# Kernel tuning notes

Hardware: AMD Instinct MI355X
Metric: run time of the kernel (lower is better)

Reference implementation:

```python
import jax, jax.numpy as jnp
import numpy as np

D_MODEL = 1024
N_HEADS = 16
HEAD_DIM = D_MODEL // N_HEADS
D_FF = 4 * D_MODEL


def _layernorm(x, g, b, eps=1e-5):
    mu = jnp.mean(x, axis=-1, keepdims=True)
    var = jnp.var(x, axis=-1, keepdims=True)
    return (x - mu) * jax.lax.rsqrt(var + eps) * g + b


def setup_inputs() -> dict:
    key = jax.random.key(0)
    ks = jax.random.split(key, 12)
    s = lambda fan_in: 1.0 / np.sqrt(fan_in)
    x = jax.random.normal(ks[0], (2, 2048, D_MODEL), dtype=jnp.float32)
    return {
        "x": x,
        "ln1_g": jnp.ones((D_MODEL,), jnp.float32),
        "ln1_b": jnp.zeros((D_MODEL,), jnp.float32),
        "w_qkv": jax.random.uniform(ks[1], (D_MODEL, 3 * D_MODEL), jnp.float32, -s(D_MODEL), s(D_MODEL)),
        "b_qkv": jax.random.uniform(ks[2], (3 * D_MODEL,), jnp.float32, -s(D_MODEL), s(D_MODEL)),
        "w_out": jax.random.uniform(ks[3], (D_MODEL, D_MODEL), jnp.float32, -s(D_MODEL), s(D_MODEL)),
        "b_out": jax.random.uniform(ks[4], (D_MODEL,), jnp.float32, -s(D_MODEL), s(D_MODEL)),
        "ln2_g": jnp.ones((D_MODEL,), jnp.float32),
        "ln2_b": jnp.zeros((D_MODEL,), jnp.float32),
        "w_ff1": jax.random.uniform(ks[5], (D_MODEL, D_FF), jnp.float32, -s(D_MODEL), s(D_MODEL)),
        "b_ff1": jax.random.uniform(ks[6], (D_FF,), jnp.float32, -s(D_MODEL), s(D_MODEL)),
        "w_ff2": jax.random.uniform(ks[7], (D_FF, D_MODEL), jnp.float32, -s(D_FF), s(D_FF)),
        "b_ff2": jax.random.uniform(ks[8], (D_MODEL,), jnp.float32, -s(D_FF), s(D_FF)),
    }


def reference(x, ln1_g, ln1_b, w_qkv, b_qkv, w_out, b_out,
              ln2_g, ln2_b, w_ff1, b_ff1, w_ff2, b_ff2):
    B, T, C = x.shape
    # --- pre-LN causal self-attention + residual ---
    h = _layernorm(x, ln1_g, ln1_b)
    qkv = h @ w_qkv + b_qkv                                  # [B,T,3C]
    qkv = qkv.reshape(B, T, 3, N_HEADS, HEAD_DIM)
    q, k, v = qkv[:, :, 0], qkv[:, :, 1], qkv[:, :, 2]       # [B,T,H,Dh]
    scores = jnp.einsum("bthd,bshd->bhts", q, k) / np.sqrt(HEAD_DIM).astype(np.float32)
    causal = jnp.tril(jnp.ones((T, T), dtype=bool))
    scores = jnp.where(causal, scores, -jnp.inf)
    weights = jax.nn.softmax(scores, axis=-1)                # [B,H,T,T]
    attn = jnp.einsum("bhts,bshd->bthd", weights, v).reshape(B, T, C)
    x = x + attn @ w_out + b_out
    # --- pre-LN GELU FFN + residual ---
    h = _layernorm(x, ln2_g, ln2_b)
    h = jax.nn.gelu(h @ w_ff1 + b_ff1, approximate=False)    # torch GELU = erf
    x = x + h @ w_ff2 + b_ff2
    return x
```

## Files before the change

### kernel.cpp

```cpp
#include <hip/hip_runtime.h>
#include <hip/hip_bf16.h>
#include <math.h>

#define TSEQ 2048
#define BATCH 2
#define CDIM 1024
#define NH 16
#define HD 64
#define DFF 4096
#define ROWS (BATCH*TSEQ)

typedef __attribute__((ext_vector_type(4))) float f32x4;
typedef __attribute__((ext_vector_type(8))) short bf16x8;
typedef __attribute__((ext_vector_type(4))) unsigned short u16x4;

__device__ __forceinline__ void gload_lds16(const void* g, void* l) {
    void* gv = const_cast<void*>(g);
    __builtin_amdgcn_global_load_lds((__attribute__((address_space(1))) void*)gv,
                                     (__attribute__((address_space(3))) void*)l, 16, 0, 0);
}

__device__ __forceinline__ unsigned short f2bf(float f) {
    unsigned int u = __float_as_uint(f);
    return (unsigned short)((u + 0x7FFFu + ((u >> 16) & 1u)) >> 16);
}
__device__ __forceinline__ float bf2f(unsigned short u) {
    return __uint_as_float((unsigned int)u << 16);
}
__device__ __forceinline__ unsigned int cvt_pk_bf16(float lo, float hi) {
    unsigned int r;
    asm("v_cvt_pk_bf16_f32 %0, %1, %2" : "=v"(r) : "v"(lo), "v"(hi));
    return r;
}
__device__ __forceinline__ float fast_gelu(float v) {
    float u = fmaf(0.044715f * v * v, v, v);
    float e = __expf(-1.5957691216057308f * u);
    return v * __builtin_amdgcn_rcpf(1.0f + e);
}

__global__ __launch_bounds__(256) void ln_kernel(const float* __restrict__ x,
                                                 const float* __restrict__ g,
                                                 const float* __restrict__ b,
                                                 unsigned short* __restrict__ out) {
    int row = blockIdx.x;
    int tid = threadIdx.x;
    const float* xr = x + (size_t)row * CDIM;
    float4 v = *(const float4*)(xr + tid * 4);
    float s  = v.x + v.y + v.z + v.w;
    float s2 = v.x*v.x + v.y*v.y + v.z*v.z + v.w*v.w;
    #pragma unroll
    for (int off = 32; off >= 1; off >>= 1) {
        s  += __shfl_down(s, off);
        s2 += __shfl_down(s2, off);
    }
    __shared__ float red[8];
    int wid = tid >> 6, lane = tid & 63;
    if (lane == 0) { red[wid] = s; red[wid + 4] = s2; }
    __syncthreads();
    float ts  = red[0] + red[1] + red[2] + red[3];
    float ts2 = red[4] + red[5] + red[6] + red[7];
    float mu  = ts * (1.0f / CDIM);
    float var = ts2 * (1.0f / CDIM) - mu * mu;
    float rstd = rsqrtf(var + 1e-5f);
    float4 gv = *(const float4*)(g + tid * 4);
    float4 bv = *(const float4*)(b + tid * 4);
    unsigned short o4[4];
    o4[0] = f2bf((v.x - mu) * rstd * gv.x + bv.x);
    o4[1] = f2bf((v.y - mu) * rstd * gv.y + bv.y);
    o4[2] = f2bf((v.z - mu) * rstd * gv.z + bv.z);
    o4[3] = f2bf((v.w - mu) * rstd * gv.w + bv.w);
    *(u16x4*)(out + (size_t)row * CDIM + tid * 4) = *(u16x4*)o4;
}

__global__ __launch_bounds__(256) void prep_kernel(
        const float* __restrict__ w_qkv, const float* __restrict__ w_out,
        const float* __restrict__ w_ff1, const float* __restrict__ w_ff2,
        const float* __restrict__ x, const float* __restrict__ ln1_g,
        const float* __restrict__ ln1_b,
        unsigned short* __restrict__ wqkvT, unsigned short* __restrict__ woutT,
        unsigned short* __restrict__ wff1T, unsigned short* __restrict__ wff2T,
        unsigned short* __restrict__ h_bf) {
    __shared__ float T[64][65];
    __shared__ float red[8];
    int bid = blockIdx.x;
    int tid = threadIdx.x;

    if (bid >= 3072) {
        const int row = bid - 3072;
        const float* xr = x + (size_t)row * CDIM;
        float4 v = *(const float4*)(xr + tid * 4);
        float s  = v.x + v.y + v.z + v.w;
        float s2 = v.x*v.x + v.y*v.y + v.z*v.z + v.w*v.w;
        #pragma unroll
        for (int off = 32; off >= 1; off >>= 1) {
            s  += __shfl_down(s, off);
            s2 += __shfl_down(s2, off);
        }
        int wid = tid >> 6, lane = tid & 63;
        if (lane == 0) { red[wid] = s; red[wid + 4] = s2; }
        __syncthreads();
        float ts  = red[0] + red[1] + red[2] + red[3];
        float ts2 = red[4] + red[5] + red[6] + red[7];
        float mu  = ts * (1.0f / CDIM);
        float var = ts2 * (1.0f / CDIM) - mu * mu;
        float rstd = rsqrtf(var + 1e-5f);
        float4 gv = *(const float4*)(ln1_g + tid * 4);
        float4 bv = *(const float4*)(ln1_b + tid * 4);
        unsigned short o4[4];
        o4[0] = f2bf((v.x - mu) * rstd * gv.x + bv.x);
        o4[1] = f2bf((v.y - mu) * rstd * gv.y + bv.y);
        o4[2] = f2bf((v.z - mu) * rstd * gv.z + bv.z);
        o4[3] = f2bf((v.w - mu) * rstd * gv.w + bv.w);
        *(u16x4*)(h_bf + (size_t)row * CDIM + tid * 4) = *(u16x4*)o4;
        return;
    }

    const float* W; unsigned short* Wt; int K, N, nbx;
    if (bid < 768)       {             W = w_qkv; Wt = wqkvT; K = 1024; N = 3072; nbx = 48; }
    else if (bid < 1024) { bid -= 768;  W = w_out; Wt = woutT; K = 1024; N = 1024; nbx = 16; }
    else if (bid < 2048) { bid -= 1024; W = w_ff1; Wt = wff1T; K = 1024; N = 4096; nbx = 64; }
    else                 { bid -= 2048; W = w_ff2; Wt = wff2T; K = 4096; N = 1024; nbx = 16; }
    const int n0 = (bid % nbx) * 64, k0 = (bid / nbx) * 64;

    int kr = tid >> 4;
    int nc = (tid & 15) * 4;
    #pragma unroll
    for (int i = 0; i < 4; ++i) {
        float4 v = *(const float4*)&W[(size_t)(k0 + kr + i*16) * N + (n0 + nc)];
        T[kr + i*16][nc + 0] = v.x;
        T[kr + i*16][nc + 1] = v.y;
        T[kr + i*16][nc + 2] = v.z;
        T[kr + i*16][nc + 3] = v.w;
    }
    __syncthreads();
    int n  = tid >> 2;
    int kb = (tid & 3) * 16;
    unsigned short tmp[16];
    #pragma unroll
    for (int i = 0; i < 16; ++i) tmp[i] = f2bf(T[kb + i][n]);
    unsigned short* dst = Wt + (size_t)(n0 + n) * K + (k0 + kb);
    *(int4*)dst       = *(int4*)&tmp[0];
    *(int4*)(dst + 8) = *(int4*)&tmp[8];
}

template<int EPI>
__global__ __launch_bounds__(512) void gemm_kernel(const unsigned short* __restrict__ A,
                                                   const unsigned short* __restrict__ Bt,
                                                   const float* __restrict__ bias,
                                                   const float* __restrict__ res,
                                                   void* __restrict__ Cout,
                                                   unsigned short* __restrict__ kfrag_,
                                                   unsigned short* __restrict__ vfrag_,
                                                   int M, int N, int K,
                                                   int nxc, int xcw, int xrw) {
    __shared__ __align__(16) unsigned short As[3 * 8192];
    __shared__ __align__(16) unsigned short Bs[3 * 8192];
    const int tid = threadIdx.x;
    const int l   = tid & 63;
    const int w   = tid >> 6;
    const int wr  = (w >> 2) * 128;
    const int wcl = (w & 3) * 64;
    const int lin = blockIdx.x;
    const int xcd = lin & 7;
    const int idx = lin >> 3;
    const int xc  = xcd % nxc, xr = xcd / nxc;
    const long brow = (long)(xr * xrw + idx / xcw) * 256;
    const long bcol = (long)(xc * xcw + idx % xcw) * 256;

    const int srow = tid >> 2;
    const int schk = ((tid & 3) ^ ((srow >> 1) & 3)) * 8;
    const unsigned short* gA = A  + (size_t)(brow + srow) * K + schk;
    const unsigned short* gB = Bt + (size_t)(bcol + srow) * K + schk;

    f32x4 acc[8][4];
    #pragma unroll
    for (int m = 0; m < 8; ++m)
        #pragma unroll
        for (int n = 0; n < 4; ++n) acc[m][n] = (f32x4){0.f, 0.f, 0.f, 0.f};

    #define STAGE256(buf, koff_)                                                       \
        do {                                                                           \
            unsigned short* lA_ = As + (buf) * 8192 + tid * 8;                         \
            unsigned short* lB_ = Bs + (buf) * 8192 + tid * 8;                         \
            gload_lds16(gA + (koff_), lA_);                                            \
            gload_lds16(gA + (size_t)128 * K + (koff_), lA_ + 4096);                   \
            gload_lds16(gB + (koff_), lB_);                                            \
            gload_lds16(gB + (size_t)128 * K + (koff_), lB_ + 4096);                   \
        } while (0)

    STAGE256(0, 0);
    STAGE256(1, 32);

    int cur = 0;
    for (int k0 = 0; k0 < K; k0 += 32) {
        if (k0 + 32 < K) asm volatile("s_waitcnt vmcnt(4)" ::: "memory");
        else             asm volatile("s_waitcnt vmcnt(0)" ::: "memory");
        __builtin_amdgcn_s_barrier();
        asm volatile("" ::: "memory");

        const unsigned short* cA = As + cur * 8192;
        const unsigned short* cB = Bs + cur * 8192;
        const int koff = ((l >> 4) ^ (((l & 15) >> 1) & 3)) * 8;
        bf16x8 af[8], bf[4];
        #pragma unroll
        for (int m = 0; m < 8; ++m)
            af[m] = *(const bf16x8*)&cA[(wr + m * 16 + (l & 15)) * 32 + koff];
        #pragma unroll
        for (int n = 0; n < 4; ++n)
            bf[n] = *(const bf16x8*)&cB[(wcl + n * 16 + (l & 15)) * 32 + koff];
        __builtin_amdgcn_s_setprio(1);
        #pragma unroll
        for (int m = 0; m < 8; ++m)
            #pragma unroll
            for (int n = 0; n < 4; ++n)
                acc[m][n] = __builtin_amdgcn_mfma_f32_16x16x32_bf16(af[m], bf[n], acc[m][n], 0, 0, 0);
        __builtin_amdgcn_s_setprio(0);

        if (k0 + 64 < K) {
            int nxt = cur + 2; if (nxt >= 3) nxt -= 3;
            STAGE256(nxt, k0 + 64);
        }
        cur = cur + 1; if (cur == 3) cur = 0;
    }
    #undef STAGE256

    const int reg = (int)(bcol >> 10);
    #pragma unroll
    for (int m = 0; m < 8; ++m) {
        const int rown = wr + m * 16 + (l >> 4) * 4;
        #pragma unroll
        for (int n = 0; n < 4; ++n) {
            const long col = bcol + wcl + n * 16 + (l & 15);
            const float bb = bias[col];
            #pragma unroll
            for (int r = 0; r < 4; ++r) {
                const long row = brow + rown + r;
                float v = acc[m][n][r] + bb;
                if (EPI == 1) {
                    v += res[row * N + col];
                    ((float*)Cout)[row * N + col] = v;
                } else if (EPI == 2) {
                    ((unsigned short*)Cout)[row * N + col] = f2bf(fast_gelu(v));
                } else if (EPI == 3) {
                    const unsigned short bv = f2bf(v);
                    if (reg == 0) {
                        ((unsigned short*)Cout)[row * 1024 + col] = bv;
                    } else {
                        const int dfull = (int)col - reg * 1024;
                        const int hh = dfull >> 6, dd = dfull & 63;
                        const int bb2 = (int)(row >> 11), tt = (int)(row & 2047);
                        const int jj = tt >> 6;
                        const size_t tb = ((size_t)((bb2 * 16 + hh) * 32 + jj)) * 8;
                        if (reg == 1) {
                            const int sb2 = (tt >> 4) & 3, llo = tt & 15;
                            const int gg2 = dd >> 5, lhi = (dd >> 3) & 3, ii = dd & 7;
                            kfrag_[(tb + sb2 * 2 + gg2) * 512 + (lhi * 16 + llo) * 8 + ii] = bv;
                        } else {
                            const int kb2 = (tt >> 5) & 1, lhi = (tt >> 3) & 3, ii = tt & 7;
                            const int db2 = dd >> 4, llo = dd & 15;
                            vfrag_[(tb + kb2 * 4 + db2) * 512 + (lhi * 16 + llo) * 8 + ii] = bv;
                        }
                    }
                } else {
                    ((unsigned short*)Cout)[row * N + col] = f2bf(v);
                }
            }
        }
    }
}

template<int EPI>
__global__ __launch_bounds__(512) void gemmsk_kernel(const unsigned short* __restrict__ A,
                                                     const unsigned short* __restrict__ Bt,
                                                     const float* __restrict__ bias,
                                                     const float* __restrict__ res,
                                                     void* __restrict__ Cout,
                                                     int M, int N, int K,
                                                     int nxc, int xcw, int xrw) {
    __shared__ __align__(16) unsigned short smem[6 * 8192];
    unsigned short* As = smem;
    unsigned short* Bs = smem + 3 * 8192;
    const int tid = threadIdx.x;
    const int l   = tid & 63;
    const int w   = tid >> 6;
    const int ks  = w >> 2;
    const int wr  = ((w >> 1) & 1) * 64;
    const int wc  = (w & 1) * 64;
    const int lin = blockIdx.x;
    const int xcd = lin & 7;
    const int idx = lin >> 3;
    const int xc  = xcd % nxc, xr = xcd / nxc;
    const long brow = (long)(xr * xrw + idx / xcw) * 128;
    const long bcol = (long)(xc * xcw + idx % xcw) * 128;

    const int srow = tid >> 3;
    const int schk = ((tid & 7) ^ (srow & 7)) * 8;
    const unsigned short* gA = A  + (size_t)(brow + srow) * K + schk;
    const unsigned short* gB = Bt + (size_t)(bcol + srow) * K + schk;

    f32x4 acc[4][4];
    #pragma unroll
    for (int m = 0; m < 4; ++m)
        #pragma unroll
        for (int n = 0; n < 4; ++n) acc[m][n] = (f32x4){0.f, 0.f, 0.f, 0.f};

    #define STAGESK(buf, koff_)                                                        \
        do {                                                                           \
            unsigned short* lA_ = As + (buf) * 8192 + tid * 8;                         \
            unsigned short* lB_ = Bs + (buf) * 8192 + tid * 8;                         \
            gload_lds16(gA + (koff_), lA_);                                            \
            gload_lds16(gA + (size_t)64 * K + (koff_), lA_ + 4096);                    \
            gload_lds16(gB + (koff_), lB_);                                            \
            gload_lds16(gB + (size_t)64 * K + (koff_), lB_ + 4096);                    \
        } while (0)

    STAGESK(0, 0);
    STAGESK(1, 64);

    int cur = 0, t = 0;
    for (int k0 = 0; k0 < K; k0 += 64, ++t) {
        if (k0 + 64 < K) asm volatile("s_waitcnt vmcnt(4)" ::: "memory");
        else             asm volatile("s_waitcnt vmcnt(0)" ::: "memory");
        __builtin_amdgcn_s_barrier();
        asm volatile("" ::: "memory");

        if ((t & 1) == ks) {
            const unsigned short* cA = As + cur * 8192;
            const unsigned short* cB = Bs + cur * 8192;
            #pragma unroll
            for (int gg = 0; gg < 2; ++gg) {
                const int koff = ((gg * 4 + (l >> 4)) ^ (l & 7)) * 8;
                bf16x8 af[4], bf[4];
                #pragma unroll
                for (int m = 0; m < 4; ++m)
                    af[m] = *(const bf16x8*)&cA[(wr + m * 16 + (l & 15)) * 64 + koff];
                #pragma unroll
                for (int n = 0; n < 4; ++n)
                    bf[n] = *(const bf16x8*)&cB[(wc + n * 16 + (l & 15)) * 64 + koff];
                __builtin_amdgcn_s_setprio(1);
                #pragma unroll
                for (int m = 0; m < 4; ++m)
                    #pragma unroll
                    for (int n = 0; n < 4; ++n)
                        acc[m][n] = __builtin_amdgcn_mfma_f32_16x16x32_bf16(af[m], bf[n], acc[m][n], 0, 0, 0);
                __builtin_amdgcn_s_setprio(0);
            }
        }

        if (k0 + 128 < K) {
            int nxt = cur + 2; if (nxt >= 3) nxt -= 3;
            STAGESK(nxt, k0 + 128);
        }
        cur = cur + 1; if (cur == 3) cur = 0;
    }
    #undef STAGESK

    __syncthreads();
    float* red = (float*)smem;
    const int rgn = w & 3;
    if (ks == 1) {
        #pragma unroll
        for (int m = 0; m < 4; ++m)
            #pragma unroll
            for (int n = 0; n < 4; ++n)
                *(f32x4*)&red[rgn * 4096 + l * 64 + ((m * 4 + n) ^ (l & 15)) * 4] = acc[m][n];
    }
    __syncthreads();
    if (ks == 1) return;

    #pragma unroll
    for (int m = 0; m < 4; ++m)
        #pragma unroll
        for (int n = 0; n < 4; ++n) {
            f32x4 p = *(const f32x4*)&red[rgn * 4096 + l * 64 + ((m * 4 + n) ^ (l & 15)) * 4];
            acc[m][n] += p;
        }

    #pragma unroll
    for (int m = 0; m < 4; ++m) {
        const int rown = wr + m * 16 + (l >> 4) * 4;
        #pragma unroll
        for (int n = 0; n < 4; ++n) {
            const long col = bcol + wc + n * 16 + (l & 15);
            const float bb = bias[col];
            #pragma unroll
            for (int r = 0; r < 4; ++r) {
                const long row = brow + rown + r;
                float v = acc[m][n][r] + bb;
                if (EPI == 1) {
                    v += res[row * N + col];
                    ((float*)Cout)[row * N + col] = v;
                } else if (EPI == 2) {
                    ((unsigned short*)Cout)[row * N + col] = f2bf(fast_gelu(v));
                } else {
                    ((unsigned short*)Cout)[row * N + col] = f2bf(v);
                }
            }
        }
    }
}

#define QSCALE 0.18033688011112042f
#define RTHR 8.0f
__global__ __launch_bounds__(64) void attn_kernel(const unsigned short* __restrict__ qbuf,
                                                  const unsigned short* __restrict__ kfrag,
                                                  const unsigned short* __restrict__ vfrag,
                                                  unsigned short* __restrict__ out) {
    __shared__ __align__(16) unsigned short Ps[16 * 128];

    const int l    = threadIdx.x;
    const int q    = l & 15;
    const int g    = l >> 4;
    const int lin  = blockIdx.x;
    const int xcd  = lin & 7;
    const int rest = lin >> 3;
    const int h    = xcd + 8 * (rest & 1);
    const int b    = (rest >> 1) & 1;
    const int strip = 127 - (rest >> 2);
    const int jmax  = strip >> 2;
    const size_t rowbase = (size_t)b * TSEQ;
    const int bh = b * NH + h;
    const int qglob = strip * 16 + q;

    const unsigned short* kfb = kfrag + (size_t)bh * 32 * 8 * 512;
    const unsigned short* vfb = vfrag + (size_t)bh * 32 * 8 * 512;

    bf16x8 aq0, aq1;
    {
        const unsigned short* qp = qbuf + (rowbase + qglob) * 1024 + h * 64 + g * 8;
        bf16x8 t0 = *(const bf16x8*)qp;
        bf16x8 t1 = *(const bf16x8*)(qp + 32);
        #pragma unroll
        for (int i = 0; i < 8; ++i) {
            aq0[i] = (short)f2bf(bf2f((unsigned short)t0[i]) * QSCALE);
            aq1[i] = (short)f2bf(bf2f((unsigned short)t1[i]) * QSCALE);
        }
    }

    float mrow = -INFINITY, lrow = 0.f;
    f32x4 o[4];
    #pragma unroll
    for (int d = 0; d < 4; ++d) o[d] = (f32x4){0.f, 0.f, 0.f, 0.f};

    for (int j = 0; j + 1 <= jmax; j += 2) {
        const bool diag2 = (j + 1 == jmax);

        bf16x8 kf[16];
        #pragma unroll
        for (int t = 0; t < 2; ++t)
            #pragma unroll
            for (int sb = 0; sb < 4; ++sb) {
                const unsigned short* kp = kfb + (size_t)((j + t) * 8 + sb * 2) * 512 + l * 8;
                kf[t * 8 + sb * 2]     = *(const bf16x8*)kp;
                kf[t * 8 + sb * 2 + 1] = *(const bf16x8*)(kp + 512);
            }

        f32x4 sf[8];
        __builtin_amdgcn_s_setprio(1);
        #pragma unroll
        for (int t = 0; t < 2; ++t)
            #pragma unroll
            for (int sb = 0; sb < 4; ++sb) {
                f32x4 acc = (f32x4){0.f, 0.f, 0.f, 0.f};
                acc = __builtin_amdgcn_mfma_f32_16x16x32_bf16(kf[t*8 + sb*2],     aq0, acc, 0, 0, 0);
                acc = __builtin_amdgcn_mfma_f32_16x16x32_bf16(kf[t*8 + sb*2 + 1], aq1, acc, 0, 0, 0);
                sf[t*4 + sb] = acc;
            }
        __builtin_amdgcn_s_setprio(0);

        bf16x8 vf[16];
        #pragma unroll
        for (int kb = 0; kb < 4; ++kb)
            #pragma unroll
            for (int db = 0; db < 4; ++db)
                vf[kb * 4 + db] = *(const bf16x8*)(vfb + (size_t)((j + (kb >> 1)) * 8 + (kb & 1) * 4 + db) * 512 + l * 8);

        if (diag2) {
            #pragma unroll
            for (int sb = 0; sb < 4; ++sb) {
                const int sg = (j + 1) * 64 + sb * 16 + 4 * g;
                #pragma unroll
                for (int r = 0; r < 4; ++r)
                    if (sg + r > qglob) sf[4 + sb][r] = -INFINITY;
            }
        }

        f32x4 mv = sf[0];
        #pragma unroll
        for (int i = 1; i < 8; ++i)
            #pragma unroll
            for (int r = 0; r < 4; ++r) mv[r] = fmaxf(mv[r], sf[i][r]);
        float mloc = fmaxf(fmaxf(mv[0], mv[1]), fmaxf(mv[2], mv[3]));
        mloc = fmaxf(mloc, __shfl_xor(mloc, 16));
        mloc = fmaxf(mloc, __shfl_xor(mloc, 32));

        float mn;
        if (__all(mloc <= mrow + RTHR)) {
            mn = mrow;
        } else {
            mn = fmaxf(mrow, mloc);
            const float alpha = exp2f(mrow - mn);
            mrow = mn;
            lrow *= alpha;
            float al[4];
            #pragma unroll
            for (int r = 0; r < 4; ++r) al[r] = __shfl(alpha, g * 4 + r);
            #pragma unroll
            for (int d = 0; d < 4; ++d)
                #pragma unroll
                for (int r = 0; r < 4; ++r) o[d][r] *= al[r];
        }

        float psum = 0.f;
        #pragma unroll
        for (int i = 0; i < 8; ++i) {
            const int t = i >> 2, sb = i & 3;
            float p0 = exp2f(sf[i][0] - mn);
            float p1 = exp2f(sf[i][1] - mn);
            float p2 = exp2f(sf[i][2] - mn);
            float p3 = exp2f(sf[i][3] - mn);
            psum += (p0 + p1) + (p2 + p3);
            unsigned int pk0 = cvt_pk_bf16(p0, p1);
            unsigned int pk1 = cvt_pk_bf16(p2, p3);
            const int c16 = (t * 8 + sb * 2 + (g >> 1)) ^ (q & 7);
            *(uint2*)((char*)Ps + q * 256 + c16 * 16 + (g & 1) * 8) = make_uint2(pk0, pk1);
        }
        psum += __shfl_xor(psum, 16);
        psum += __shfl_xor(psum, 32);
        lrow += psum;

        __builtin_amdgcn_s_setprio(1);
        #pragma unroll
        for (int kb = 0; kb < 4; ++kb) {
            const int c16 = (kb * 4 + g) ^ (q & 7);
            bf16x8 pa = *(const bf16x8*)((const char*)Ps + q * 256 + c16 * 16);
            #pragma unroll
            for (int db = 0; db < 4; ++db)
                o[db] = __builtin_amdgcn_mfma_f32_16x16x32_bf16(pa, vf[kb * 4 + db], o[db], 0, 0, 0);
        }
        __builtin_amdgcn_s_setprio(0);
    }

    if ((jmax & 1) == 0) {
        const int j = jmax;
        bf16x8 kf[8];
        #pragma unroll
        for (int sb = 0; sb < 4; ++sb) {
            const unsigned short* kp = kfb + (size_t)(j * 8 + sb * 2) * 512 + l * 8;
            kf[sb * 2]     = *(const bf16x8*)kp;
            kf[sb * 2 + 1] = *(const bf16x8*)(kp + 512);
        }
        f32x4 sf[4];
        __builtin_amdgcn_s_setprio(1);
        #pragma unroll
        for (int sb = 0; sb < 4; ++sb) {
            f32x4 acc = (f32x4){0.f, 0.f, 0.f, 0.f};
            acc = __builtin_amdgcn_mfma_f32_16x16x32_bf16(kf[sb*2],     aq0, acc, 0, 0, 0);
            acc = __builtin_amdgcn_mfma_f32_16x16x32_bf16(kf[sb*2 + 1], aq1, acc, 0, 0, 0);
            sf[sb] = acc;
        }
        __builtin_amdgcn_s_setprio(0);

        bf16x8 vf[8];
        #pragma unroll
        for (int kb = 0; kb < 2; ++kb)
            #pragma unroll
            for (int db = 0; db < 4; ++db)
                vf[kb * 4 + db] = *(const bf16x8*)(vfb + (size_t)(j * 8 + kb * 4 + db) * 512 + l * 8);

        #pragma unroll
        for (int sb = 0; sb < 4; ++sb) {
            const int sg = j * 64 + sb * 16 + 4 * g;
            #pragma unroll
            for (int r = 0; r < 4; ++r)
                if (sg + r > qglob) sf[sb][r] = -INFINITY;
        }

        f32x4 mv = sf[0];
        #pragma unroll
        for (int i = 1; i < 4; ++i)
            #pragma unroll
            for (int r = 0; r < 4; ++r) mv[r] = fmaxf(mv[r], sf[i][r]);
        float mloc = fmaxf(fmaxf(mv[0], mv[1]), fmaxf(mv[2], mv[3]));
        mloc = fmaxf(mloc, __shfl_xor(mloc, 16));
        mloc = fmaxf(mloc, __shfl_xor(mloc, 32));

        float mn;
        if (__all(mloc <= mrow + RTHR)) {
            mn = mrow;
        } else {
            mn = fmaxf(mrow, mloc);
            const float alpha = exp2f(mrow - mn);
            mrow = mn;
            lrow *= alpha;
            float al[4];
            #pragma unroll
            for (int r = 0; r < 4; ++r) al[r] = __shfl(alpha, g * 4 + r);
            #pragma unroll
            for (int d = 0; d < 4; ++d)
                #pragma unroll
                for (int r = 0; r < 4; ++r) o[d][r] *= al[r];
        }

        float psum = 0.f;
        #pragma unroll
        for (int sb = 0; sb < 4; ++sb) {
            float p0 = exp2f(sf[sb][0] - mn);
            float p1 = exp2f(sf[sb][1] - mn);
            float p2 = exp2f(sf[sb][2] - mn);
            float p3 = exp2f(sf[sb][3] - mn);
            psum += (p0 + p1) + (p2 + p3);
            unsigned int pk0 = cvt_pk_bf16(p0, p1);
            unsigned int pk1 = cvt_pk_bf16(p2, p3);
            const int c16 = (sb * 2 + (g >> 1)) ^ (q & 7);
            *(uint2*)((char*)Ps + q * 256 + c16 * 16 + (g & 1) * 8) = make_uint2(pk0, pk1);
        }
        psum += __shfl_xor(psum, 16);
        psum += __shfl_xor(psum, 32);
        lrow += psum;

        __builtin_amdgcn_s_setprio(1);
        #pragma unroll
        for (int kb = 0; kb < 2; ++kb) {
            const int c16 = (kb * 4 + g) ^ (q & 7);
            bf16x8 pa = *(const bf16x8*)((const char*)Ps + q * 256 + c16 * 16);
            #pragma unroll
            for (int db = 0; db < 4; ++db)
                o[db] = __builtin_amdgcn_mfma_f32_16x16x32_bf16(pa, vf[kb * 4 + db], o[db], 0, 0, 0);
        }
        __builtin_amdgcn_s_setprio(0);
    }

    float linv[4];
    #pragma unroll
    for (int r = 0; r < 4; ++r) linv[r] = 1.0f / __shfl(lrow, g * 4 + r);
    #pragma unroll
    for (int r = 0; r < 4; ++r) {
        const size_t rb = (rowbase + strip * 16 + g * 4 + r) * (size_t)CDIM + h * 64 + q;
        #pragma unroll
        for (int d = 0; d < 4; ++d)
            out[rb + d * 16] = f2bf(o[d][r] * linv[r]);
    }
}

extern "C" void kernel_launch(void* const* d_in, const int* in_sizes, int n_in,
                              void* d_out, int out_size, void* d_ws, size_t ws_size,
                              hipStream_t stream) {
    const float* x     = (const float*)d_in[0];
    const float* ln1_g = (const float*)d_in[1];
    const float* ln1_b = (const float*)d_in[2];
    const float* w_qkv = (const float*)d_in[3];
    const float* b_qkv = (const float*)d_in[4];
    const float* w_out = (const float*)d_in[5];
    const float* b_out = (const float*)d_in[6];
    const float* ln2_g = (const float*)d_in[7];
    const float* ln2_b = (const float*)d_in[8];
    const float* w_ff1 = (const float*)d_in[9];
    const float* b_ff1 = (const float*)d_in[10];
    const float* w_ff2 = (const float*)d_in[11];
    const float* b_ff2 = (const float*)d_in[12];
    float* out = (float*)d_out;

    char* wsb = (char*)d_ws;
    unsigned short* h_bf    = (unsigned short*)(wsb);
    unsigned short* qbuf    = (unsigned short*)(wsb + 8ll  * 1024 * 1024);
    unsigned short* attn_bf = (unsigned short*)(wsb + 32ll * 1024 * 1024);
    float*          x1      = (float*)         (wsb + 40ll * 1024 * 1024);
    unsigned short* kfrag   = (unsigned short*)(wsb + 40ll * 1024 * 1024);
    unsigned short* vfrag   = (unsigned short*)(wsb + 48ll * 1024 * 1024);
    unsigned short* wqkvT   = (unsigned short*)(wsb + 56ll * 1024 * 1024);
    unsigned short* woutT   = (unsigned short*)(wsb + 62ll * 1024 * 1024);
    unsigned short* wff1T   = (unsigned short*)(wsb + 64ll * 1024 * 1024);
    unsigned short* wff2T   = (unsigned short*)(wsb + 72ll * 1024 * 1024);
    unsigned short* ff1_bf  = (unsigned short*)(wsb + 8ll  * 1024 * 1024);

    prep_kernel<<<7168, 256, 0, stream>>>(w_qkv, w_out, w_ff1, w_ff2,
                                          x, ln1_g, ln1_b,
                                          wqkvT, woutT, wff1T, wff2T, h_bf);
    gemm_kernel<3><<<192, 512, 0, stream>>>(h_bf, wqkvT, b_qkv, nullptr, qbuf,
                                            kfrag, vfrag, ROWS, 3072, 1024, 4, 3, 8);
    attn_kernel<<<4096, 64, 0, stream>>>(qbuf, kfrag, vfrag, attn_bf);
    gemmsk_kernel<1><<<256, 512, 0, stream>>>(attn_bf, woutT, b_out, x, x1,
                                              ROWS, 1024, 1024, 2, 4, 8);
    ln_kernel<<<ROWS, 256, 0, stream>>>(x1, ln2_g, ln2_b, h_bf);
    gemm_kernel<2><<<256, 512, 0, stream>>>(h_bf, wff1T, b_ff1, nullptr, ff1_bf,
                                            nullptr, nullptr, ROWS, 4096, 1024, 4, 4, 8);
    gemmsk_kernel<1><<<256, 512, 0, stream>>>(ff1_bf, wff2T, b_ff2, x1, (float*)out,
                                              ROWS, 1024, 4096, 2, 4, 8);
}
```

Before: 214.8 us.

## Process two query strips per attention wave to share K/V fragment loads

Each attention wave now handles two adjacent 16-row query strips (A and B) instead of one. The K and V fragments for a key block are loaded once and used for both strips' QK and PV MFMAs, and the grid is halved to match. The online-softmax/PV step is moved into a templated helper that is called once per strip, with the LDS P buffer reused in sequence. This cuts global K/V traffic per query row, at the cost of more registers (two accumulator sets, two score sets) and half as many waves to hide latency.

```diff
diff --git a/kernel.cpp b/kernel.cpp
--- a/kernel.cpp
+++ b/kernel.cpp
@@ -402,6 +402,66 @@
 
 #define QSCALE 0.18033688011112042f
 #define RTHR 8.0f
+
+template<int NT>
+__device__ __forceinline__ void softmax_pv(f32x4* sf, float& mrow, float& lrow,
+                                           f32x4* o, const bf16x8* vf,
+                                           unsigned short* Ps, const int q, const int g) {
+    f32x4 mv = sf[0];
+    #pragma unroll
+    for (int i = 1; i < NT * 4; ++i)
+        #pragma unroll
+        for (int r = 0; r < 4; ++r) mv[r] = fmaxf(mv[r], sf[i][r]);
+    float mloc = fmaxf(fmaxf(mv[0], mv[1]), fmaxf(mv[2], mv[3]));
+    mloc = fmaxf(mloc, __shfl_xor(mloc, 16));
+    mloc = fmaxf(mloc, __shfl_xor(mloc, 32));
+
+    float mn;
+    if (__all(mloc <= mrow + RTHR)) {
+        mn = mrow;
+    } else {
+        mn = fmaxf(mrow, mloc);
+        const float alpha = exp2f(mrow - mn);
+        mrow = mn;
+        lrow *= alpha;
+        float al[4];
+        #pragma unroll
+        for (int r = 0; r < 4; ++r) al[r] = __shfl(alpha, g * 4 + r);
+        #pragma unroll
+        for (int d = 0; d < 4; ++d)
+            #pragma unroll
+            for (int r = 0; r < 4; ++r) o[d][r] *= al[r];
+    }
+
+    float psum = 0.f;
+    #pragma unroll
+    for (int i = 0; i < NT * 4; ++i) {
+        float p0 = exp2f(sf[i][0] - mn);
+        float p1 = exp2f(sf[i][1] - mn);
+        float p2 = exp2f(sf[i][2] - mn);
+        float p3 = exp2f(sf[i][3] - mn);
+        psum += (p0 + p1) + (p2 + p3);
+        unsigned int pk0 = cvt_pk_bf16(p0, p1);
+        unsigned int pk1 = cvt_pk_bf16(p2, p3);
+        const int c16 = (i * 2 + (g >> 1)) ^ (q & 7);
+        *(uint2*)((char*)Ps + q * 256 + c16 * 16 + (g & 1) * 8) = make_uint2(pk0, pk1);
+    }
+    psum += __shfl_xor(psum, 16);
+    psum += __shfl_xor(psum, 32);
+    lrow += psum;
+
+    __builtin_amdgcn_s_setprio(1);
+    #pragma unroll
+    for (int kb = 0; kb < NT * 2; ++kb) {
+        const int c16 = (kb * 4 + g) ^ (q & 7);
+        bf16x8 pa = *(const bf16x8*)((const char*)Ps + q * 256 + c16 * 16);
+        #pragma unroll
+        for (int db = 0; db < 4; ++db)
+            o[db] = __builtin_amdgcn_mfma_f32_16x16x32_bf16(pa, vf[kb * 4 + db], o[db], 0, 0, 0);
+    }
+    __builtin_amdgcn_s_setprio(0);
+}
+
 __global__ __launch_bounds__(64) void attn_kernel(const unsigned short* __restrict__ qbuf,
                                                   const unsigned short* __restrict__ kfrag,
                                                   const unsigned short* __restrict__ vfrag,
@@ -416,31 +476,38 @@
     const int rest = lin >> 3;
     const int h    = xcd + 8 * (rest & 1);
     const int b    = (rest >> 1) & 1;
-    const int strip = 127 - (rest >> 2);
-    const int jmax  = strip >> 2;
+    const int ss     = 63 - (rest >> 2);
+    const int strip0 = ss * 2;
+    const int jmax   = ss >> 1;
     const size_t rowbase = (size_t)b * TSEQ;
     const int bh = b * NH + h;
-    const int qglob = strip * 16 + q;
+    const int qgA = strip0 * 16 + q;
+    const int qgB = qgA + 16;
 
     const unsigned short* kfb = kfrag + (size_t)bh * 32 * 8 * 512;
     const unsigned short* vfb = vfrag + (size_t)bh * 32 * 8 * 512;
 
-    bf16x8 aq0, aq1;
+    bf16x8 aqA0, aqA1, aqB0, aqB1;
     {
-        const unsigned short* qp = qbuf + (rowbase + qglob) * 1024 + h * 64 + g * 8;
-        bf16x8 t0 = *(const bf16x8*)qp;
-        bf16x8 t1 = *(const bf16x8*)(qp + 32);
+        const unsigned short* qpA = qbuf + (rowbase + qgA) * 1024 + h * 64 + g * 8;
+        const unsigned short* qpB = qpA + (size_t)16 * 1024;
+        bf16x8 t0 = *(const bf16x8*)qpA;
+        bf16x8 t1 = *(const bf16x8*)(qpA + 32);
+        bf16x8 t2 = *(const bf16x8*)qpB;
+        bf16x8 t3 = *(const bf16x8*)(qpB + 32);
         #pragma unroll
         for (int i = 0; i < 8; ++i) {
-            aq0[i] = (short)f2bf(bf2f((unsigned short)t0[i]) * QSCALE);
-            aq1[i] = (short)f2bf(bf2f((unsigned short)t1[i]) * QSCALE);
-        }
-    }
-
-    float mrow = -INFINITY, lrow = 0.f;
-    f32x4 o[4];
-    #pragma unroll
-    for (int d = 0; d < 4; ++d) o[d] = (f32x4){0.f, 0.f, 0.f, 0.f};
+            aqA0[i] = (short)f2bf(bf2f((unsigned short)t0[i]) * QSCALE);
+            aqA1[i] = (short)f2bf(bf2f((unsigned short)t1[i]) * QSCALE);
+            aqB0[i] = (short)f2bf(bf2f((unsigned short)t2[i]) * QSCALE);
+            aqB1[i] = (short)f2bf(bf2f((unsigned short)t3[i]) * QSCALE);
+        }
+    }
+
+    float mrA = -INFINITY, lrA = 0.f, mrB = -INFINITY, lrB = 0.f;
+    f32x4 oA[4], oB[4];
+    #pragma unroll
+    for (int d = 0; d < 4; ++d) { oA[d] = (f32x4){0.f,0.f,0.f,0.f}; oB[d] = (f32x4){0.f,0.f,0.f,0.f}; }
 
     for (int j = 0; j + 1 <= jmax; j += 2) {
         const bool diag2 = (j + 1 == jmax);
@@ -455,16 +522,20 @@
                 kf[t * 8 + sb * 2 + 1] = *(const bf16x8*)(kp + 512);
             }
 
-        f32x4 sf[8];
+        f32x4 sfA[8], sfB[8];
         __builtin_amdgcn_s_setprio(1);
         #pragma unroll
         for (int t = 0; t < 2; ++t)
             #pragma unroll
             for (int sb = 0; sb < 4; ++sb) {
-                f32x4 acc = (f32x4){0.f, 0.f, 0.f, 0.f};
-                acc = __builtin_amdgcn_mfma_f32_16x16x32_bf16(kf[t*8 + sb*2],     aq0, acc, 0, 0, 0);
-                acc = __builtin_amdgcn_mfma_f32_16x16x32_bf16(kf[t*8 + sb*2 + 1], aq1, acc, 0, 0, 0);
-                sf[t*4 + sb] = acc;
+                f32x4 a = (f32x4){0.f, 0.f, 0.f, 0.f};
+                a = __builtin_amdgcn_mfma_f32_16x16x32_bf16(kf[t*8 + sb*2],     aqA0, a, 0, 0, 0);
+                a = __builtin_amdgcn_mfma_f32_16x16x32_bf16(kf[t*8 + sb*2 + 1], aqA1, a, 0, 0, 0);
+                sfA[t*4 + sb] = a;
+                f32x4 c = (f32x4){0.f, 0.f, 0.f, 0.f};
+                c = __builtin_amdgcn_mfma_f32_16x16x32_bf16(kf[t*8 + sb*2],     aqB0, c, 0, 0, 0);
+                c = __builtin_amdgcn_mfma_f32_16x16x32_bf16(kf[t*8 + sb*2 + 1], aqB1, c, 0, 0, 0);
+                sfB[t*4 + sb] = c;
             }
         __builtin_amdgcn_s_setprio(0);
 
@@ -480,65 +551,15 @@
             for (int sb = 0; sb < 4; ++sb) {
                 const int sg = (j + 1) * 64 + sb * 16 + 4 * g;
                 #pragma unroll
-                for (int r = 0; r < 4; ++r)
-                    if (sg + r > qglob) sf[4 + sb][r] = -INFINITY;
+                for (int r = 0; r < 4; ++r) {
+                    if (sg + r > qgA) sfA[4 + sb][r] = -INFINITY;
+                    if (sg + r > qgB) sfB[4 + sb][r] = -INFINITY;
+                }
             }
         }
 
-        f32x4 mv = sf[0];
-        #pragma unroll
-        for (int i = 1; i < 8; ++i)
-            #pragma unroll
-            for (int r = 0; r < 4; ++r) mv[r] = fmaxf(mv[r], sf[i][r]);
-        float mloc = fmaxf(fmaxf(mv[0], mv[1]), fmaxf(mv[2], mv[3]));
-        mloc = fmaxf(mloc, __shfl_xor(mloc, 16));
-        mloc = fmaxf(mloc, __shfl_xor(mloc, 32));
-
-        float mn;
-        if (__all(mloc <= mrow + RTHR)) {
-            mn = mrow;
-        } else {
-            mn = fmaxf(mrow, mloc);
-            const float alpha = exp2f(mrow - mn);
-            mrow = mn;
-            lrow *= alpha;
-            float al[4];
-            #pragma unroll
-            for (int r = 0; r < 4; ++r) al[r] = __shfl(alpha, g * 4 + r);
-            #pragma unroll
-            for (int d = 0; d < 4; ++d)
-                #pragma unroll
-                for (int r = 0; r < 4; ++r) o[d][r] *= al[r];
-        }
-
-        float psum = 0.f;
-        #pragma unroll
-        for (int i = 0; i < 8; ++i) {
-            const int t = i >> 2, sb = i & 3;
-            float p0 = exp2f(sf[i][0] - mn);
-            float p1 = exp2f(sf[i][1] - mn);
-            float p2 = exp2f(sf[i][2] - mn);
-            float p3 = exp2f(sf[i][3] - mn);
-            psum += (p0 + p1) + (p2 + p3);
-            unsigned int pk0 = cvt_pk_bf16(p0, p1);
-            unsigned int pk1 = cvt_pk_bf16(p2, p3);
-            const int c16 = (t * 8 + sb * 2 + (g >> 1)) ^ (q & 7);
-            *(uint2*)((char*)Ps + q * 256 + c16 * 16 + (g & 1) * 8) = make_uint2(pk0, pk1);
-        }
-        psum += __shfl_xor(psum, 16);
-        psum += __shfl_xor(psum, 32);
-        lrow += psum;
-
-        __builtin_amdgcn_s_setprio(1);
-        #pragma unroll
-        for (int kb = 0; kb < 4; ++kb) {
-            const int c16 = (kb * 4 + g) ^ (q & 7);
-            bf16x8 pa = *(const bf16x8*)((const char*)Ps + q * 256 + c16 * 16);
-            #pragma unroll
-            for (int db = 0; db < 4; ++db)
-                o[db] = __builtin_amdgcn_mfma_f32_16x16x32_bf16(pa, vf[kb * 4 + db], o[db], 0, 0, 0);
-        }
-        __builtin_amdgcn_s_setprio(0);
+        softmax_pv<2>(sfA, mrA, lrA, oA, vf, Ps, q, g);
+        softmax_pv<2>(sfB, mrB, lrB, oB, vf, Ps, q, g);
     }
 
     if ((jmax & 1) == 0) {
@@ -550,14 +571,18 @@
             kf[sb * 2]     = *(const bf16x8*)kp;
             kf[sb * 2 + 1] = *(const bf16x8*)(kp + 512);
         }
-        f32x4 sf[4];
+        f32x4 sfA[4], sfB[4];
         __builtin_amdgcn_s_setprio(1);
         #pragma unroll
         for (int sb = 0; sb < 4; ++sb) {
-            f32x4 acc = (f32x4){0.f, 0.f, 0.f, 0.f};
-            acc = __builtin_amdgcn_mfma_f32_16x16x32_bf16(kf[sb*2],     aq0, acc, 0, 0, 0);
-            acc = __builtin_amdgcn_mfma_f32_16x16x32_bf16(kf[sb*2 + 1], aq1, acc, 0, 0, 0);
-            sf[sb] = acc;
+            f32x4 a = (f32x4){0.f, 0.f, 0.f, 0.f};
+            a = __builtin_amdgcn_mfma_f32_16x16x32_bf16(kf[sb*2],     aqA0, a, 0, 0, 0);
+            a = __builtin_amdgcn_mfma_f32_16x16x32_bf16(kf[sb*2 + 1], aqA1, a, 0, 0, 0);
+            sfA[sb] = a;
+            f32x4 c = (f32x4){0.f, 0.f, 0.f, 0.f};
+            c = __builtin_amdgcn_mfma_f32_16x16x32_bf16(kf[sb*2],     aqB0, c, 0, 0, 0);
+            c = __builtin_amdgcn_mfma_f32_16x16x32_bf16(kf[sb*2 + 1], aqB1, c, 0, 0, 0);
+            sfB[sb] = c;
         }
         __builtin_amdgcn_s_setprio(0);
 
@@ -572,74 +597,31 @@
         for (int sb = 0; sb < 4; ++sb) {
             const int sg = j * 64 + sb * 16 + 4 * g;
             #pragma unroll
-            for (int r = 0; r < 4; ++r)
-                if (sg + r > qglob) sf[sb][r] = -INFINITY;
-        }
-
-        f32x4 mv = sf[0];
-        #pragma unroll
-        for (int i = 1; i < 4; ++i)
-            #pragma unroll
-            for (int r = 0; r < 4; ++r) mv[r] = fmaxf(mv[r], sf[i][r]);
-        float mloc = fmaxf(fmaxf(mv[0], mv[1]), fmaxf(mv[2], mv[3]));
-        mloc = fmaxf(mloc, __shfl_xor(mloc, 16));
-        mloc = fmaxf(mloc, __shfl_xor(mloc, 32));
-
-        float mn;
-        if (__all(mloc <= mrow + RTHR)) {
-            mn = mrow;
-        } else {
-            mn = fmaxf(mrow, mloc);
-            const float alpha = exp2f(mrow - mn);
-            mrow = mn;
-            lrow *= alpha;
-            float al[4];
-            #pragma unroll
-            for (int r = 0; r < 4; ++r) al[r] = __shfl(alpha, g * 4 + r);
-            #pragma unroll
-            for (int d = 0; d < 4; ++d)
-                #pragma unroll
-                for (int r = 0; r < 4; ++r) o[d][r] *= al[r];
-        }
-
-        float psum = 0.f;
-        #pragma unroll
-        for (int sb = 0; sb < 4; ++sb) {
-            float p0 = exp2f(sf[sb][0] - mn);
-            float p1 = exp2f(sf[sb][1] - mn);
-            float p2 = exp2f(sf[sb][2] - mn);
-            float p3 = exp2f(sf[sb][3] - mn);
-            psum += (p0 + p1) + (p2 + p3);
-            unsigned int pk0 = cvt_pk_bf16(p0, p1);
-            unsigned int pk1 = cvt_pk_bf16(p2, p3);
-            const int c16 = (sb * 2 + (g >> 1)) ^ (q & 7);
-            *(uint2*)((char*)Ps + q * 256 + c16 * 16 + (g & 1) * 8) = make_uint2(pk0, pk1);
-        }
-        psum += __shfl_xor(psum, 16);
-        psum += __shfl_xor(psum, 32);
-        lrow += psum;
-
-        __builtin_amdgcn_s_setprio(1);
-        #pragma unroll
-        for (int kb = 0; kb < 2; ++kb) {
-            const int c16 = (kb * 4 + g) ^ (q & 7);
-            bf16x8 pa = *(const bf16x8*)((const char*)Ps + q * 256 + c16 * 16);
-            #pragma unroll
-            for (int db = 0; db < 4; ++db)
-                o[db] = __builtin_amdgcn_mfma_f32_16x16x32_bf16(pa, vf[kb * 4 + db], o[db], 0, 0, 0);
-        }
-        __builtin_amdgcn_s_setprio(0);
-    }
-
-    float linv[4];
-    #pragma unroll
-    for (int r = 0; r < 4; ++r) linv[r] = 1.0f / __shfl(lrow, g * 4 + r);
+            for (int r = 0; r < 4; ++r) {
+                if (sg + r > qgA) sfA[sb][r] = -INFINITY;
+                if (sg + r > qgB) sfB[sb][r] = -INFINITY;
+            }
+        }
+
+        softmax_pv<1>(sfA, mrA, lrA, oA, vf, Ps, q, g);
+        softmax_pv<1>(sfB, mrB, lrB, oB, vf, Ps, q, g);
+    }
+
+    float linvA[4], linvB[4];
     #pragma unroll
     for (int r = 0; r < 4; ++r) {
-        const size_t rb = (rowbase + strip * 16 + g * 4 + r) * (size_t)CDIM + h * 64 + q;
-        #pragma unroll
-        for (int d = 0; d < 4; ++d)
-            out[rb + d * 16] = f2bf(o[d][r] * linv[r]);
+        linvA[r] = 1.0f / __shfl(lrA, g * 4 + r);
+        linvB[r] = 1.0f / __shfl(lrB, g * 4 + r);
+    }
+    #pragma unroll
+    for (int r = 0; r < 4; ++r) {
+        const size_t rbA = (rowbase + strip0 * 16 + g * 4 + r) * (size_t)CDIM + h * 64 + q;
+        const size_t rbB = rbA + (size_t)16 * CDIM;
+        #pragma unroll
+        for (int d = 0; d < 4; ++d) {
+            out[rbA + d * 16] = f2bf(oA[d][r] * linvA[r]);
+            out[rbB + d * 16] = f2bf(oB[d][r] * linvB[r]);
+        }
     }
 }
 
@@ -679,7 +661,7 @@
                                           wqkvT, woutT, wff1T, wff2T, h_bf);
     gemm_kernel<3><<<192, 512, 0, stream>>>(h_bf, wqkvT, b_qkv, nullptr, qbuf,
                                             kfrag, vfrag, ROWS, 3072, 1024, 4, 3, 8);
-    attn_kernel<<<4096, 64, 0, stream>>>(qbuf, kfrag, vfrag, attn_bf);
+    attn_kernel<<<2048, 64, 0, stream>>>(qbuf, kfrag, vfrag, attn_bf);
     gemmsk_kernel<1><<<256, 512, 0, stream>>>(attn_bf, woutT, b_out, x, x1,
                                               ROWS, 1024, 1024, 2, 4, 8);
     ln_kernel<<<ROWS, 256, 0, stream>>>(x1, ln2_g, ln2_b, h_bf);
```

New measurement: 219.6 us. +2.2%, slower.
